# Kernel optimization log

Measured on AMD Instinct MI355X. Metric: run time of the kernel, lower is better.

Reference implementation:

```python
import jax, jax.numpy as jnp
import numpy as np
from math import sqrt

SEQ, NIN, NH, NOUT, HEADS = 4096, 1024, 128, 1024, 8
DOUT = HEADS * (2 * NH + NOUT)  # 10240
EPS = 1e-5

def setup_inputs() -> dict:
    key = jax.random.key(0)
    k1, k2, k3 = jax.random.split(key, 3)
    x = jax.random.normal(k1, (SEQ, NIN), dtype=jnp.float32)
    W = jax.random.normal(k2, (DOUT, NIN), dtype=jnp.float32) * (1.0 / sqrt(NIN))
    b = jax.random.normal(k3, (DOUT,), dtype=jnp.float32) * 0.01
    ln_w = jnp.ones((NOUT,), dtype=jnp.float32)
    ln_b = jnp.zeros((NOUT,), dtype=jnp.float32)
    return {"x": x, "W": W, "b": b, "ln_w": ln_w, "ln_b": ln_b}

def reference(x, W, b, ln_w, ln_b):
    # fused QKV projection: (S, NIN) -> (S, HEADS, 2*NH + NOUT)
    out = (x @ W.T + b).reshape(x.shape[0], HEADS, -1)
    keys, queries, values = jnp.split(out, (NH, 2 * NH), axis=-1)
    keys = keys / sqrt(keys.shape[-1])
    # logits[i, j, h] = sum_k keys[i,h,k] * queries[j,h,k]
    logits = jnp.einsum('ihk,jhk->ijh', keys, queries)
    attention = jax.nn.softmax(logits, axis=1)
    # sum over j and heads -> (S, NOUT)
    output = jnp.einsum('ijh,jhe->ie', attention, values)
    # LayerNorm over last dim, elementwise affine, eps=1e-5
    mean = jnp.mean(output, axis=-1, keepdims=True)
    var = jnp.var(output, axis=-1, keepdims=True)
    normed = (output - mean) / jnp.sqrt(var + EPS)
    return normed * ln_w + ln_b
```

## Files before the change

### kernel.cpp

```cpp
#include <hip/hip_runtime.h>

typedef __attribute__((ext_vector_type(8))) __bf16 bf16x8;
typedef __attribute__((ext_vector_type(4))) __bf16 bf16x4;
typedef __attribute__((ext_vector_type(4))) float f32x4;
typedef __attribute__((ext_vector_type(16))) float f32x16;

#define SEQ   4096
#define NIN   1024
#define DH    128
#define NOUTD 1024
#define HEADS 8
#define CPH   1280
#define L2E   1.44269504f
#define KTOT  32768

static __device__ inline f32x16 zero16() {
  f32x16 z;
#pragma unroll
  for (int r = 0; r < 16; ++r) z[r] = 0.f;
  return z;
}

static __device__ inline unsigned pk2(float a, float b) {
  unsigned short ua = __builtin_bit_cast(unsigned short, (__bf16)a);
  unsigned short ub = __builtin_bit_cast(unsigned short, (__bf16)b);
  return (unsigned)ua | ((unsigned)ub << 16);
}

__global__ __launch_bounds__(256) void k_cvt(const float* __restrict__ src,
                                             __bf16* __restrict__ dst, int n) {
  int i = (blockIdx.x * 256 + threadIdx.x) * 4;
  if (i >= n) return;
  float4 v = *(const float4*)(src + i);
  bf16x4 o = { (__bf16)v.x, (__bf16)v.y, (__bf16)v.z, (__bf16)v.w };
  *(bf16x4*)(dst + i) = o;
}

__global__ __launch_bounds__(256) void k_zero(float4* __restrict__ p) {
  p[(size_t)blockIdx.x * 256 + threadIdx.x] = float4{0.f, 0.f, 0.f, 0.f};
}

__global__ __launch_bounds__(256) void k_gemm_qkv(
    const __bf16* __restrict__ xb, const __bf16* __restrict__ wb,
    const float* __restrict__ bias,
    __bf16* __restrict__ Kx, __bf16* __restrict__ Q2, __bf16* __restrict__ Vd,
    int vmode)
{
  __shared__ __align__(16) __bf16 As[128 * 32];
  __shared__ __align__(16) __bf16 Bs[128 * 32];
  const int tid = threadIdx.x;
  const int w = tid >> 6, l = tid & 63;
  const int i0 = blockIdx.x * 128;
  const int n0 = blockIdx.y * 128;
  const int lrow = l & 15;
  const int lkb  = (l >> 4) * 16;
  const int soff = (w * 2) * 1024 + l * 16;

  f32x4 acc[4][4] = {};

  for (int kt = 0; kt < 32; ++kt) {
    __syncthreads();
#pragma unroll
    for (int q = 0; q < 2; ++q) {
      int off = soff + q * 1024;
      int row = off >> 6, kb = off & 63;
      const __bf16* ga = xb + (size_t)(i0 + row) * NIN + kt * 32 + (kb >> 1);
      const __bf16* gb = wb + (size_t)(n0 + row) * NIN + kt * 32 + (kb >> 1);
      __builtin_amdgcn_global_load_lds(
          (const __attribute__((address_space(1))) void*)ga,
          (__attribute__((address_space(3))) void*)((char*)As + (w * 2 + q) * 1024),
          16, 0, 0);
      __builtin_amdgcn_global_load_lds(
          (const __attribute__((address_space(1))) void*)gb,
          (__attribute__((address_space(3))) void*)((char*)Bs + (w * 2 + q) * 1024),
          16, 0, 0);
    }
    __syncthreads();
    bf16x8 af[4], bfr[4];
#pragma unroll
    for (int mi = 0; mi < 4; ++mi)
      af[mi] = *(const bf16x8*)((const char*)As + (((w >> 1) * 64 + mi * 16 + lrow) * 64) + lkb);
#pragma unroll
    for (int ni = 0; ni < 4; ++ni)
      bfr[ni] = *(const bf16x8*)((const char*)Bs + (((w & 1) * 64 + ni * 16 + lrow) * 64) + lkb);
#pragma unroll
    for (int mi = 0; mi < 4; ++mi)
#pragma unroll
      for (int ni = 0; ni < 4; ++ni)
        acc[mi][ni] = __builtin_amdgcn_mfma_f32_16x16x32_bf16(af[mi], bfr[ni], acc[mi][ni], 0, 0, 0);
  }

  const int iw = i0 + (w >> 1) * 64;
  const int nw = n0 + (w & 1) * 64;
  const int lhi = l >> 4;
#pragma unroll
  for (int ni = 0; ni < 4; ++ni) {
    int n = nw + ni * 16 + lrow;
    float bv = bias[n];
    int h = n / CPH;
    int c = n - h * CPH;
    if (c < 128) {
#pragma unroll
      for (int mi = 0; mi < 4; ++mi)
#pragma unroll
        for (int r = 0; r < 4; ++r) {
          int i = iw + mi * 16 + lhi * 4 + r;
          float v = acc[mi][ni][r] + bv;
          Kx[(((size_t)h * SEQ + i) << 7) + c] = (__bf16)(v * 0.08838834764831845f);
        }
    } else if (c < 256) {
      int d = c - 128;
      size_t qEl = ((size_t)(h * 16 + (d >> 3)) << 15) + (size_t)(d & 7);
#pragma unroll
      for (int mi = 0; mi < 4; ++mi)
#pragma unroll
        for (int r = 0; r < 4; ++r) {
          int j = iw + mi * 16 + lhi * 4 + r;
          Q2[qEl + ((size_t)j << 3)] = (__bf16)(acc[mi][ni][r] + bv);
        }
    } else {
      int e = c - 256;
      bf16x4 pk = { (__bf16)(acc[0][ni][0]), (__bf16)(0.f), (__bf16)(0.f), (__bf16)(0.f) };
#pragma unroll
      for (int mi = 0; mi < 4; ++mi) {
        int jb = iw + mi * 16 + lhi * 4;
        pk = bf16x4{ (__bf16)(acc[mi][ni][0] + bv), (__bf16)(acc[mi][ni][1] + bv),
                     (__bf16)(acc[mi][ni][2] + bv), (__bf16)(acc[mi][ni][3] + bv) };
        if (vmode) {
          *(bf16x4*)(Vd + (size_t)e * KTOT + (size_t)h * SEQ + jb) = pk;
        } else {
          int J = jb >> 3, js = jb & 7;
          *(bf16x4*)(Vd + (((size_t)(h * 512 + J)) << 13) + ((size_t)e << 3) + js) = pk;
        }
      }
    }
  }
}

__global__ __launch_bounds__(256) void k_stats(
    const __bf16* __restrict__ Kx, const __bf16* __restrict__ Q2,
    float* __restrict__ stat_m, float* __restrict__ stat_il)
{
  __shared__ __align__(16) char Qb[2][16384];
  const int tid = threadIdx.x;
  const int w = tid >> 6, l = tid & 63;
  const int l31 = l & 31, hl = l >> 5;
  const int b = blockIdx.x;
  const int h = b >> 5;
  const int i_base = (b & 31) * 128;
  const __bf16* Kh = Kx + ((size_t)h * SEQ << 7);
  const char* q2b = (const char*)Q2 + ((size_t)h << 20);

  bf16x8 kf[8];
#pragma unroll
  for (int c = 0; c < 8; ++c)
    kf[c] = *(const bf16x8*)(Kh + (((size_t)(i_base + 32 * w + l31)) << 7) + c * 16 + hl * 8);

  float m_run = -1e30f, l_run = 0.f;

#pragma unroll
  for (int k = 0; k < 4; ++k) {
    int s = tid + k * 256;
    const char* src = q2b + ((size_t)(s >> 6) << 16) + (size_t)(s & 63) * 16;
    __builtin_amdgcn_global_load_lds(
        (const __attribute__((address_space(1))) void*)src,
        (__attribute__((address_space(3))) void*)(Qb[0] + s * 16), 16, 0, 0);
  }
  __syncthreads();

  for (int jt = 0; jt < 64; ++jt) {
    const int cur = jt & 1;
    if (jt < 63) {
      int j0n = (jt + 1) * 64;
#pragma unroll
      for (int k = 0; k < 4; ++k) {
        int s = tid + k * 256;
        const char* src = q2b + ((size_t)(s >> 6) << 16) + (size_t)(j0n + (s & 63)) * 16;
        __builtin_amdgcn_global_load_lds(
            (const __attribute__((address_space(1))) void*)src,
            (__attribute__((address_space(3))) void*)(Qb[cur ^ 1] + s * 16), 16, 0, 0);
      }
    }
    const char* qb = Qb[cur];

    f32x16 s0 = zero16(), s1 = zero16();
#pragma unroll
    for (int c = 0; c < 8; ++c) {
      bf16x8 a0 = *(const bf16x8*)(qb + (((2 * c + hl) * 64 + l31) << 4));
      bf16x8 a1 = *(const bf16x8*)(qb + (((2 * c + hl) * 64 + 32 + l31) << 4));
      s0 = __builtin_amdgcn_mfma_f32_32x32x16_bf16(a0, kf[c], s0, 0, 0, 0);
      s1 = __builtin_amdgcn_mfma_f32_32x32x16_bf16(a1, kf[c], s1, 0, 0, 0);
    }

    float pm = -1e30f;
#pragma unroll
    for (int r = 0; r < 16; ++r) pm = fmaxf(pm, fmaxf(s0[r], s1[r]));
    float mn = fmaxf(m_run, pm);
    l_run *= exp2f((m_run - mn) * L2E);
    float a = 0.f;
#pragma unroll
    for (int r = 0; r < 16; ++r)
      a += exp2f((s0[r] - mn) * L2E) + exp2f((s1[r] - mn) * L2E);
    l_run += a;
    m_run = mn;
    __syncthreads();
  }

  float mp = __shfl_xor(m_run, 32);
  float lp = __shfl_xor(l_run, 32);
  float mf = fmaxf(m_run, mp);
  float lf = l_run * exp2f((m_run - mf) * L2E) + lp * exp2f((mp - mf) * L2E);
  if (hl == 0) {
    int i = i_base + 32 * w + l31;
    stat_m[h * SEQ + i] = mf;
    stat_il[h * SEQ + i] = 1.0f / lf;
  }
}

__global__ __launch_bounds__(256) void k_pwrite(
    const __bf16* __restrict__ Kx, const __bf16* __restrict__ Q2,
    const float* __restrict__ stat_m, const float* __restrict__ stat_il,
    __bf16* __restrict__ P)
{
  __shared__ __align__(16) char Qb[2][16384];
  const int tid = threadIdx.x;
  const int w = tid >> 6, l = tid & 63;
  const int l31 = l & 31, hl = l >> 5;
  const int b = blockIdx.x;
  const int h = b >> 5;
  const int i_base = (b & 31) * 128;
  const __bf16* Kh = Kx + ((size_t)h * SEQ << 7);
  const char* q2b = (const char*)Q2 + ((size_t)h << 20);

  const int i = i_base + 32 * w + l31;
  const float m_i = stat_m[h * SEQ + i];
  const float il_i = stat_il[h * SEQ + i];
  __bf16* prow = P + ((size_t)i << 15) + (size_t)h * SEQ;

  bf16x8 kf[8];
#pragma unroll
  for (int c = 0; c < 8; ++c)
    kf[c] = *(const bf16x8*)(Kh + (((size_t)i) << 7) + c * 16 + hl * 8);

#pragma unroll
  for (int k = 0; k < 4; ++k) {
    int s = tid + k * 256;
    const char* src = q2b + ((size_t)(s >> 6) << 16) + (size_t)(s & 63) * 16;
    __builtin_amdgcn_global_load_lds(
        (const __attribute__((address_space(1))) void*)src,
        (__attribute__((address_space(3))) void*)(Qb[0] + s * 16), 16, 0, 0);
  }
  __syncthreads();

  for (int jt = 0; jt < 64; ++jt) {
    const int cur = jt & 1;
    if (jt < 63) {
      int j0n = (jt + 1) * 64;
#pragma unroll
      for (int k = 0; k < 4; ++k) {
        int s = tid + k * 256;
        const char* src = q2b + ((size_t)(s >> 6) << 16) + (size_t)(j0n + (s & 63)) * 16;
        __builtin_amdgcn_global_load_lds(
            (const __attribute__((address_space(1))) void*)src,
            (__attribute__((address_space(3))) void*)(Qb[cur ^ 1] + s * 16), 16, 0, 0);
      }
    }
    const char* qb = Qb[cur];

    f32x16 s0 = zero16(), s1 = zero16();
#pragma unroll
    for (int c = 0; c < 8; ++c) {
      bf16x8 a0 = *(const bf16x8*)(qb + (((2 * c + hl) * 64 + l31) << 4));
      bf16x8 a1 = *(const bf16x8*)(qb + (((2 * c + hl) * 64 + 32 + l31) << 4));
      s0 = __builtin_amdgcn_mfma_f32_32x32x16_bf16(a0, kf[c], s0, 0, 0, 0);
      s1 = __builtin_amdgcn_mfma_f32_32x32x16_bf16(a1, kf[c], s1, 0, 0, 0);
    }

#pragma unroll
    for (int c2 = 0; c2 < 4; ++c2) {
      const f32x16& sv = (c2 >> 1) ? s1 : s0;
      const int base = (c2 & 1) * 8;
      float e0 = il_i * exp2f((sv[base + 0] - m_i) * L2E);
      float e1 = il_i * exp2f((sv[base + 1] - m_i) * L2E);
      float e2 = il_i * exp2f((sv[base + 2] - m_i) * L2E);
      float e3 = il_i * exp2f((sv[base + 3] - m_i) * L2E);
      float e4 = il_i * exp2f((sv[base + 4] - m_i) * L2E);
      float e5 = il_i * exp2f((sv[base + 5] - m_i) * L2E);
      float e6 = il_i * exp2f((sv[base + 6] - m_i) * L2E);
      float e7 = il_i * exp2f((sv[base + 7] - m_i) * L2E);
      unsigned WA0 = pk2(e0, e1), WA1 = pk2(e2, e3);
      unsigned WB0 = pk2(e4, e5), WB1 = pk2(e6, e7);
      unsigned send0 = hl ? WA0 : WB0;
      unsigned send1 = hl ? WA1 : WB1;
      unsigned r0 = (unsigned)__shfl_xor((int)send0, 32);
      unsigned r1 = (unsigned)__shfl_xor((int)send1, 32);
      int4 qd;
      qd.x = (int)(hl ? r0 : WA0);
      qd.y = (int)(hl ? r1 : WA1);
      qd.z = (int)(hl ? WB0 : r0);
      qd.w = (int)(hl ? WB1 : r1);
      *(int4*)(prow + jt * 64 + 16 * c2 + 8 * hl) = qd;
    }
    __syncthreads();
  }
}

__global__ __launch_bounds__(256) void k_pv_gemm(
    const __bf16* __restrict__ P, const __bf16* __restrict__ VT,
    float* __restrict__ out)
{
  __shared__ __align__(16) __bf16 As[128 * 32];
  __shared__ __align__(16) __bf16 Bs[128 * 32];
  const int tid = threadIdx.x;
  const int w = tid >> 6, l = tid & 63;
  const int i0 = blockIdx.y * 128;
  const int n0 = blockIdx.x * 128;
  const int lrow = l & 15;
  const int lkb  = (l >> 4) * 16;
  const int soff = (w * 2) * 1024 + l * 16;

  f32x4 acc[4][4] = {};

  for (int kt = 0; kt < 1024; ++kt) {
    __syncthreads();
#pragma unroll
    for (int q = 0; q < 2; ++q) {
      int off = soff + q * 1024;
      int row = off >> 6, kb = off & 63;
      const __bf16* ga = P  + (size_t)(i0 + row) * KTOT + kt * 32 + (kb >> 1);
      const __bf16* gb = VT + (size_t)(n0 + row) * KTOT + kt * 32 + (kb >> 1);
      __builtin_amdgcn_global_load_lds(
          (const __attribute__((address_space(1))) void*)ga,
          (__attribute__((address_space(3))) void*)((char*)As + (w * 2 + q) * 1024),
          16, 0, 0);
      __builtin_amdgcn_global_load_lds(
          (const __attribute__((address_space(1))) void*)gb,
          (__attribute__((address_space(3))) void*)((char*)Bs + (w * 2 + q) * 1024),
          16, 0, 0);
    }
    __syncthreads();
    bf16x8 af[4], bfr[4];
#pragma unroll
    for (int mi = 0; mi < 4; ++mi)
      af[mi] = *(const bf16x8*)((const char*)As + (((w >> 1) * 64 + mi * 16 + lrow) * 64) + lkb);
#pragma unroll
    for (int ni = 0; ni < 4; ++ni)
      bfr[ni] = *(const bf16x8*)((const char*)Bs + (((w & 1) * 64 + ni * 16 + lrow) * 64) + lkb);
#pragma unroll
    for (int mi = 0; mi < 4; ++mi)
#pragma unroll
      for (int ni = 0; ni < 4; ++ni)
        acc[mi][ni] = __builtin_amdgcn_mfma_f32_16x16x32_bf16(af[mi], bfr[ni], acc[mi][ni], 0, 0, 0);
  }

  const int iw = i0 + (w >> 1) * 64;
  const int nw = n0 + (w & 1) * 64;
  const int lhi = l >> 4;
#pragma unroll
  for (int ni = 0; ni < 4; ++ni) {
    int e = nw + ni * 16 + lrow;
#pragma unroll
    for (int mi = 0; mi < 4; ++mi)
#pragma unroll
      for (int r = 0; r < 4; ++r) {
        int i = iw + mi * 16 + lhi * 4 + r;
        out[((size_t)i << 10) + e] = acc[mi][ni][r];
      }
  }
}

__global__ __launch_bounds__(512, 2) void k_attn3(
    const __bf16* __restrict__ Kx, const __bf16* __restrict__ Q2,
    const __bf16* __restrict__ V2, const float* __restrict__ stat_m,
    const float* __restrict__ stat_il, float* __restrict__ out)
{
  __shared__ __align__(16) char Qb[2][8192];
  __shared__ __align__(16) char Vb[2][16384];
  __shared__ float s_linv[256];

  const int tid = threadIdx.x;
  const int w = tid >> 6, l = tid & 63;
  const int l31 = l & 31, hl = l >> 5;
  const int islot = w & 3, eslot = w >> 2;

  const int b = blockIdx.x;
  const int et = b & 3;
  const int h = ((b >> 2) & 1) + 2 * (b >> 7);
  const int it = (b >> 3) & 15;
  const int i_base = it * 256, e_base = et * 256;

  const __bf16* Kh = Kx + ((size_t)h * SEQ << 7);
  const char* q2b = (const char*)Q2 + ((size_t)h << 20);
  const char* v2b = (const char*)V2 + ((size_t)(h * 512) << 14) + ((size_t)e_base << 4);

  if (tid < 256) s_linv[tid] = stat_il[h * SEQ + i_base + tid];
  const int iw0 = i_base + islot * 64;
  const float m0 = stat_m[h * SEQ + iw0 + l31];
  const float m1 = stat_m[h * SEQ + iw0 + 32 + l31];

  bf16x8 kf[2][8];
#pragma unroll
  for (int ig = 0; ig < 2; ++ig)
#pragma unroll
    for (int c = 0; c < 8; ++c)
      kf[ig][c] = *(const bf16x8*)(Kh + (((size_t)(iw0 + ig * 32 + l31)) << 7) + c * 16 + hl * 8);

  f32x16 acc[2][4];
#pragma unroll
  for (int ig = 0; ig < 2; ++ig)
#pragma unroll
    for (int n = 0; n < 4; ++n) acc[ig][n] = zero16();

  {
    const char* srcQ = q2b + ((size_t)(tid >> 5) << 16) + (size_t)(tid & 31) * 16;
    __builtin_amdgcn_global_load_lds(
        (const __attribute__((address_space(1))) void*)srcQ,
        (__attribute__((address_space(3))) void*)(Qb[0] + tid * 16), 16, 0, 0);
#pragma unroll
    for (int k = 0; k < 2; ++k) {
      int s = tid + k * 512;
      const char* srcV = v2b + ((size_t)(s >> 8) << 14) + (size_t)(s & 255) * 16;
      __builtin_amdgcn_global_load_lds(
          (const __attribute__((address_space(1))) void*)srcV,
          (__attribute__((address_space(3))) void*)(Vb[0] + s * 16), 16, 0, 0);
    }
  }
  __syncthreads();

  for (int jt = 0; jt < 128; ++jt) {
    const int cur = jt & 1;
    if (jt < 127) {
      const int j0n = (jt + 1) * 32;
      const char* srcQ = q2b + ((size_t)(tid >> 5) << 16) + (size_t)(j0n + (tid & 31)) * 16;
      __builtin_amdgcn_global_load_lds(
          (const __attribute__((address_space(1))) void*)srcQ,
          (__attribute__((address_space(3))) void*)(Qb[cur ^ 1] + tid * 16), 16, 0, 0);
#pragma unroll
      for (int k = 0; k < 2; ++k) {
        int s = tid + k * 512;
        const char* srcV = v2b + ((size_t)((jt + 1) * 4 + (s >> 8)) << 14) + (size_t)(s & 255) * 16;
        __builtin_amdgcn_global_load_lds(
            (const __attribute__((address_space(1))) void*)srcV,
            (__attribute__((address_space(3))) void*)(Vb[cur ^ 1] + s * 16), 16, 0, 0);
      }
    }
    const char* qb = Qb[cur];
    const char* vb = Vb[cur];

    f32x16 s0 = zero16(), s1 = zero16();
#pragma unroll
    for (int c = 0; c < 8; ++c) {
      bf16x8 a0 = *(const bf16x8*)(qb + (((2 * c + hl) * 32 + l31) << 4));
      s0 = __builtin_amdgcn_mfma_f32_32x32x16_bf16(a0, kf[0][c], s0, 0, 0, 0);
      s1 = __builtin_amdgcn_mfma_f32_32x32x16_bf16(a0, kf[1][c], s1, 0, 0, 0);
    }

    bf16x8 pf[2][2];
#pragma unroll
    for (int ig = 0; ig < 2; ++ig) {
      const f32x16& sv = ig ? s1 : s0;
      const float mi = ig ? m1 : m0;
#pragma unroll
      for (int c2 = 0; c2 < 2; ++c2) {
        const int base = 8 * c2;
        float e0 = exp2f((sv[base + 0] - mi) * L2E);
        float e1 = exp2f((sv[base + 1] - mi) * L2E);
        float e2 = exp2f((sv[base + 2] - mi) * L2E);
        float e3 = exp2f((sv[base + 3] - mi) * L2E);
        float e4 = exp2f((sv[base + 4] - mi) * L2E);
        float e5 = exp2f((sv[base + 5] - mi) * L2E);
        float e6 = exp2f((sv[base + 6] - mi) * L2E);
        float e7 = exp2f((sv[base + 7] - mi) * L2E);
        unsigned WA0 = pk2(e0, e1), WA1 = pk2(e2, e3);
        unsigned WB0 = pk2(e4, e5), WB1 = pk2(e6, e7);
        unsigned send0 = hl ? WA0 : WB0;
        unsigned send1 = hl ? WA1 : WB1;
        unsigned r0 = (unsigned)__shfl_xor((int)send0, 32);
        unsigned r1 = (unsigned)__shfl_xor((int)send1, 32);
        int4 qd;
        qd.x = (int)(hl ? r0 : WA0);
        qd.y = (int)(hl ? r1 : WA1);
        qd.z = (int)(hl ? WB0 : r0);
        qd.w = (int)(hl ? WB1 : r1);
        pf[ig][c2] = __builtin_bit_cast(bf16x8, qd);
      }
    }

#pragma unroll
    for (int c2 = 0; c2 < 2; ++c2)
#pragma unroll
      for (int n = 0; n < 4; ++n) {
        bf16x8 bv = *(const bf16x8*)(vb + (((2 * c2 + hl) * 256 + eslot * 128 + 32 * n + l31) << 4));
        acc[0][n] = __builtin_amdgcn_mfma_f32_32x32x16_bf16(pf[0][c2], bv, acc[0][n], 0, 0, 0);
        acc[1][n] = __builtin_amdgcn_mfma_f32_32x32x16_bf16(pf[1][c2], bv, acc[1][n], 0, 0, 0);
      }
    __syncthreads();
  }

#pragma unroll
  for (int ig = 0; ig < 2; ++ig)
#pragma unroll
    for (int n = 0; n < 4; ++n) {
      const int e = e_base + eslot * 128 + 32 * n + l31;
#pragma unroll
      for (int r = 0; r < 16; ++r) {
        int row = (r & 3) + 8 * (r >> 2) + 4 * hl;
        int iloc = islot * 64 + ig * 32 + row;
        float v = acc[ig][n][r] * s_linv[iloc];
        atomicAdd(out + (((size_t)(i_base + iloc)) << 10) + e, v);
      }
    }
}

__global__ __launch_bounds__(256) void k_ln(float* __restrict__ io,
                                            const float* __restrict__ lw,
                                            const float* __restrict__ lb) {
  const int i = blockIdx.x, t = threadIdx.x;
  const int w = t >> 6, l = t & 63;
  float4 v = *(const float4*)(io + ((size_t)i << 10) + t * 4);
  float s = v.x + v.y + v.z + v.w;
  float q = v.x * v.x + v.y * v.y + v.z * v.z + v.w * v.w;
#pragma unroll
  for (int d = 1; d < 64; d <<= 1) {
    s += __shfl_xor(s, d);
    q += __shfl_xor(q, d);
  }
  __shared__ float red[4][2];
  if (l == 0) { red[w][0] = s; red[w][1] = q; }
  __syncthreads();
  s = red[0][0] + red[1][0] + red[2][0] + red[3][0];
  q = red[0][1] + red[1][1] + red[2][1] + red[3][1];
  float mean = s * (1.0f / 1024.0f);
  float var = q * (1.0f / 1024.0f) - mean * mean;
  float rstd = rsqrtf(var + 1e-5f);
  float4 gw = *(const float4*)(lw + t * 4);
  float4 gb = *(const float4*)(lb + t * 4);
  float4 ov;
  ov.x = (v.x - mean) * rstd * gw.x + gb.x;
  ov.y = (v.y - mean) * rstd * gw.y + gb.y;
  ov.z = (v.z - mean) * rstd * gw.z + gb.z;
  ov.w = (v.w - mean) * rstd * gw.w + gb.w;
  *(float4*)(io + ((size_t)i << 10) + t * 4) = ov;
}

extern "C" void kernel_launch(void* const* d_in, const int* in_sizes, int n_in,
                              void* d_out, int out_size, void* d_ws, size_t ws_size,
                              hipStream_t stream) {
  (void)in_sizes; (void)n_in; (void)out_size;
  const float* x  = (const float*)d_in[0];
  const float* W  = (const float*)d_in[1];
  const float* b  = (const float*)d_in[2];
  const float* lw = (const float*)d_in[3];
  const float* lb = (const float*)d_in[4];
  float* out = (float*)d_out;
  char* ws = (char*)d_ws;

  __bf16* xb = (__bf16*)ws;
  __bf16* wb = (__bf16*)(ws + (size_t)8  * 1024 * 1024);
  __bf16* Kx = (__bf16*)(ws + (size_t)28 * 1024 * 1024);
  __bf16* Q2 = (__bf16*)(ws + (size_t)36 * 1024 * 1024);
  __bf16* Vd = (__bf16*)(ws + (size_t)44 * 1024 * 1024);
  __bf16* P  = (__bf16*)(ws + (size_t)108 * 1024 * 1024);
  float* stat_m  = (float*)ws;
  float* stat_il = (float*)(ws + (size_t)128 * 1024);

  const bool gemm_path = ws_size >= ((size_t)364 << 20);

  k_cvt<<<4096, 256, 0, stream>>>(x, xb, SEQ * NIN);
  k_cvt<<<10240, 256, 0, stream>>>(W, wb, HEADS * CPH * NIN);
  k_gemm_qkv<<<dim3(32, 80), 256, 0, stream>>>(xb, wb, b, Kx, Q2, Vd,
                                               gemm_path ? 1 : 0);
  k_stats<<<256, 256, 0, stream>>>(Kx, Q2, stat_m, stat_il);
  if (gemm_path) {
    k_pwrite<<<256, 256, 0, stream>>>(Kx, Q2, stat_m, stat_il, P);
    k_pv_gemm<<<dim3(8, 32), 256, 0, stream>>>(P, Vd, out);
  } else {
    k_zero<<<4096, 256, 0, stream>>>((float4*)out);
    k_attn3<<<512, 512, 0, stream>>>(Kx, Q2, Vd, stat_m, stat_il, out);
  }
  k_ln<<<4096, 256, 0, stream>>>(out, lw, lb);
}
```

Before: 1.012 ms.

## Chunk P materialization by heads and rows to fit smaller workspaces

Makes the P-write kernel and the PV GEMM take head, row-chunk and j-split parameters so the probability matrix can be built and consumed in chunks. The host chooses a chunk size from the available workspace and accumulates across head chunks into the output with a beta flag. This lets the GEMM path run when the workspace is too small for the full P buffer, instead of falling back to the fused attention kernel. It also splits k_pwrite along j so there are more blocks. The costs are extra launches and read-modify-write of the output when heads are chunked.

```diff
diff --git a/kernel.cpp b/kernel.cpp
--- a/kernel.cpp
+++ b/kernel.cpp
@@ -120,12 +120,11 @@
         }
     } else {
       int e = c - 256;
-      bf16x4 pk = { (__bf16)(acc[0][ni][0]), (__bf16)(0.f), (__bf16)(0.f), (__bf16)(0.f) };
 #pragma unroll
       for (int mi = 0; mi < 4; ++mi) {
         int jb = iw + mi * 16 + lhi * 4;
-        pk = bf16x4{ (__bf16)(acc[mi][ni][0] + bv), (__bf16)(acc[mi][ni][1] + bv),
-                     (__bf16)(acc[mi][ni][2] + bv), (__bf16)(acc[mi][ni][3] + bv) };
+        bf16x4 pk = { (__bf16)(acc[mi][ni][0] + bv), (__bf16)(acc[mi][ni][1] + bv),
+                      (__bf16)(acc[mi][ni][2] + bv), (__bf16)(acc[mi][ni][3] + bv) };
         if (vmode) {
           *(bf16x4*)(Vd + (size_t)e * KTOT + (size_t)h * SEQ + jb) = pk;
         } else {
@@ -220,41 +219,49 @@
 __global__ __launch_bounds__(256) void k_pwrite(
     const __bf16* __restrict__ Kx, const __bf16* __restrict__ Q2,
     const float* __restrict__ stat_m, const float* __restrict__ stat_il,
-    __bf16* __restrict__ P)
+    __bf16* __restrict__ P, int h0, int i0, int nit, int njs, int njt, int ldP)
 {
   __shared__ __align__(16) char Qb[2][16384];
   const int tid = threadIdx.x;
   const int w = tid >> 6, l = tid & 63;
   const int l31 = l & 31, hl = l >> 5;
-  const int b = blockIdx.x;
-  const int h = b >> 5;
-  const int i_base = (b & 31) * 128;
+
+  const int bb = blockIdx.x;
+  const int js = bb % njs;
+  const int rem = bb / njs;
+  const int itile = rem % nit;
+  const int hh = rem / nit;
+  const int h = h0 + hh;
+  const int jt0 = js * njt;
+
   const __bf16* Kh = Kx + ((size_t)h * SEQ << 7);
   const char* q2b = (const char*)Q2 + ((size_t)h << 20);
 
-  const int i = i_base + 32 * w + l31;
-  const float m_i = stat_m[h * SEQ + i];
-  const float il_i = stat_il[h * SEQ + i];
-  __bf16* prow = P + ((size_t)i << 15) + (size_t)h * SEQ;
+  const int i_loc = itile * 128 + 32 * w + l31;
+  const int i_gl = i0 + i_loc;
+  const float m_i = stat_m[h * SEQ + i_gl];
+  const float il_i = stat_il[h * SEQ + i_gl];
+  __bf16* prow = P + (size_t)i_loc * ldP + (size_t)hh * SEQ;
 
   bf16x8 kf[8];
 #pragma unroll
   for (int c = 0; c < 8; ++c)
-    kf[c] = *(const bf16x8*)(Kh + (((size_t)i) << 7) + c * 16 + hl * 8);
+    kf[c] = *(const bf16x8*)(Kh + (((size_t)i_gl) << 7) + c * 16 + hl * 8);
 
 #pragma unroll
   for (int k = 0; k < 4; ++k) {
     int s = tid + k * 256;
-    const char* src = q2b + ((size_t)(s >> 6) << 16) + (size_t)(s & 63) * 16;
+    const char* src = q2b + ((size_t)(s >> 6) << 16) + (size_t)(jt0 * 64 + (s & 63)) * 16;
     __builtin_amdgcn_global_load_lds(
         (const __attribute__((address_space(1))) void*)src,
         (__attribute__((address_space(3))) void*)(Qb[0] + s * 16), 16, 0, 0);
   }
   __syncthreads();
 
-  for (int jt = 0; jt < 64; ++jt) {
-    const int cur = jt & 1;
-    if (jt < 63) {
+  for (int t = 0; t < njt; ++t) {
+    const int jt = jt0 + t;
+    const int cur = t & 1;
+    if (t < njt - 1) {
       int j0n = (jt + 1) * 64;
 #pragma unroll
       for (int k = 0; k < 4; ++k) {
@@ -307,13 +314,13 @@
 
 __global__ __launch_bounds__(256) void k_pv_gemm(
     const __bf16* __restrict__ P, const __bf16* __restrict__ VT,
-    float* __restrict__ out)
+    float* __restrict__ out, int ldP, int k0, int kiters, int i0, int beta)
 {
   __shared__ __align__(16) __bf16 As[128 * 32];
   __shared__ __align__(16) __bf16 Bs[128 * 32];
   const int tid = threadIdx.x;
   const int w = tid >> 6, l = tid & 63;
-  const int i0 = blockIdx.y * 128;
+  const int iblk = blockIdx.y * 128;
   const int n0 = blockIdx.x * 128;
   const int lrow = l & 15;
   const int lkb  = (l >> 4) * 16;
@@ -321,14 +328,14 @@
 
   f32x4 acc[4][4] = {};
 
-  for (int kt = 0; kt < 1024; ++kt) {
+  for (int kt = 0; kt < kiters; ++kt) {
     __syncthreads();
 #pragma unroll
     for (int q = 0; q < 2; ++q) {
       int off = soff + q * 1024;
       int row = off >> 6, kb = off & 63;
-      const __bf16* ga = P  + (size_t)(i0 + row) * KTOT + kt * 32 + (kb >> 1);
-      const __bf16* gb = VT + (size_t)(n0 + row) * KTOT + kt * 32 + (kb >> 1);
+      const __bf16* ga = P  + (size_t)(iblk + row) * ldP + kt * 32 + (kb >> 1);
+      const __bf16* gb = VT + (size_t)(n0 + row) * KTOT + k0 + kt * 32 + (kb >> 1);
       __builtin_amdgcn_global_load_lds(
           (const __attribute__((address_space(1))) void*)ga,
           (__attribute__((address_space(3))) void*)((char*)As + (w * 2 + q) * 1024),
@@ -353,19 +360,33 @@
         acc[mi][ni] = __builtin_amdgcn_mfma_f32_16x16x32_bf16(af[mi], bfr[ni], acc[mi][ni], 0, 0, 0);
   }
 
-  const int iw = i0 + (w >> 1) * 64;
+  const int iw = i0 + iblk + (w >> 1) * 64;
   const int nw = n0 + (w & 1) * 64;
   const int lhi = l >> 4;
-#pragma unroll
-  for (int ni = 0; ni < 4; ++ni) {
-    int e = nw + ni * 16 + lrow;
-#pragma unroll
-    for (int mi = 0; mi < 4; ++mi)
-#pragma unroll
-      for (int r = 0; r < 4; ++r) {
-        int i = iw + mi * 16 + lhi * 4 + r;
-        out[((size_t)i << 10) + e] = acc[mi][ni][r];
-      }
+  if (beta) {
+#pragma unroll
+    for (int ni = 0; ni < 4; ++ni) {
+      int e = nw + ni * 16 + lrow;
+#pragma unroll
+      for (int mi = 0; mi < 4; ++mi)
+#pragma unroll
+        for (int r = 0; r < 4; ++r) {
+          int i = iw + mi * 16 + lhi * 4 + r;
+          out[((size_t)i << 10) + e] += acc[mi][ni][r];
+        }
+    }
+  } else {
+#pragma unroll
+    for (int ni = 0; ni < 4; ++ni) {
+      int e = nw + ni * 16 + lrow;
+#pragma unroll
+      for (int mi = 0; mi < 4; ++mi)
+#pragma unroll
+        for (int r = 0; r < 4; ++r) {
+          int i = iw + mi * 16 + lhi * 4 + r;
+          out[((size_t)i << 10) + e] = acc[mi][ni][r];
+        }
+    }
   }
 }
 
@@ -564,16 +585,38 @@
   float* stat_m  = (float*)ws;
   float* stat_il = (float*)(ws + (size_t)128 * 1024);
 
-  const bool gemm_path = ws_size >= ((size_t)364 << 20);
+  const size_t MB = (size_t)1024 * 1024;
+  const size_t avail = (ws_size > 108 * MB) ? (ws_size - 108 * MB) : 0;
+
+  int HPC = 0, mr = 4096;
+  if      (avail >= 256 * MB) HPC = 8;
+  else if (avail >= 128 * MB) HPC = 4;
+  else if (avail >=  64 * MB) HPC = 2;
+  else if (avail >=  32 * MB) HPC = 1;
+  else if (avail >=  16 * MB) { HPC = 1; mr = 2048; }
+  const bool gemm_path = (HPC > 0);
 
   k_cvt<<<4096, 256, 0, stream>>>(x, xb, SEQ * NIN);
   k_cvt<<<10240, 256, 0, stream>>>(W, wb, HEADS * CPH * NIN);
   k_gemm_qkv<<<dim3(32, 80), 256, 0, stream>>>(xb, wb, b, Kx, Q2, Vd,
                                                gemm_path ? 1 : 0);
   k_stats<<<256, 256, 0, stream>>>(Kx, Q2, stat_m, stat_il);
+
   if (gemm_path) {
-    k_pwrite<<<256, 256, 0, stream>>>(Kx, Q2, stat_m, stat_il, P);
-    k_pv_gemm<<<dim3(8, 32), 256, 0, stream>>>(P, Vd, out);
+    const int nit = mr / 128;
+    const int ldP = HPC * SEQ;
+    int njs = 256 / (nit * HPC);
+    if (njs < 1) njs = 1;
+    while (64 % njs) njs >>= 1;
+    const int njt = 64 / njs;
+    for (int i0 = 0; i0 < SEQ; i0 += mr) {
+      for (int h0 = 0; h0 < HEADS; h0 += HPC) {
+        k_pwrite<<<HPC * nit * njs, 256, 0, stream>>>(
+            Kx, Q2, stat_m, stat_il, P, h0, i0, nit, njs, njt, ldP);
+        k_pv_gemm<<<dim3(8, nit), 256, 0, stream>>>(
+            P, Vd, out, ldP, h0 * SEQ, ldP / 32, i0, h0 != 0);
+      }
+    }
   } else {
     k_zero<<<4096, 256, 0, stream>>>((float4*)out);
     k_attn3<<<512, 512, 0, stream>>>(Kx, Q2, Vd, stat_m, stat_il, out);
```

New measurement: 1.170 ms. 15.6% more time.
